# Kernel tuning notes

Hardware: AMD Instinct MI355X
Metric: run time of the kernel (lower is better)

## Reference

```python
import jax, jax.numpy as jnp
import numpy as np

EMBED_DIM = 1024
NUM_HEADS = 16
HEAD_DIM = EMBED_DIM // NUM_HEADS
SCALING = HEAD_DIM ** -0.5
W_SCALE = 0.02  # small init so exp(scores) in focused path stays finite


def setup_inputs() -> dict:
    key = jax.random.key(0)
    ks = jax.random.split(key, 12)
    B, T = 2, 2048
    hidden_states = jax.random.normal(ks[0], (B, T, EMBED_DIM), dtype=jnp.float32)
    focused_attention = jax.random.uniform(ks[1], (B, T, T), dtype=jnp.float32)
    def lin(kw, kb):
        W = jax.random.normal(kw, (EMBED_DIM, EMBED_DIM), dtype=jnp.float32) * W_SCALE
        b = jax.random.normal(kb, (EMBED_DIM,), dtype=jnp.float32) * W_SCALE
        return W, b
    Wq, bq = lin(ks[2], ks[3])
    Wk, bk = lin(ks[4], ks[5])
    Wv, bv = lin(ks[6], ks[7])
    Wo, bo = lin(ks[8], ks[9])
    return {"hidden_states": hidden_states, "focused_attention": focused_attention,
            "Wq": Wq, "bq": bq, "Wk": Wk, "bk": bk, "Wv": Wv, "bv": bv, "Wo": Wo, "bo": bo}


def reference(hidden_states, focused_attention, Wq, bq, Wk, bk, Wv, bv, Wo, bo):
    B, T, D = hidden_states.shape
    H, hd = NUM_HEADS, HEAD_DIM

    def shape_heads(x):  # [B,T,D] -> [B,H,T,hd]
        return x.reshape(B, T, H, hd).transpose(0, 2, 1, 3)

    q = shape_heads((hidden_states @ Wq.T + bq) * SCALING)
    k = shape_heads(hidden_states @ Wk.T + bk)
    v = shape_heads(hidden_states @ Wv.T + bv)

    # [B,H,T,S] raw attention logits
    scores = jnp.einsum('bhtd,bhsd->bhts', q, k)

    # focused_attention path: exp-weighted normalization (not a plain softmax)
    f = focused_attention[:, None, :, :]  # broadcast over heads
    e = f * jnp.exp(scores)
    attn = e / jnp.sum(e, axis=-1, keepdims=True)

    out = jnp.einsum('bhts,bhsd->bhtd', attn, v)  # [B,H,T,hd]
    out = out.transpose(0, 2, 1, 3).reshape(B, T, D)
    return out @ Wo.T + bo
```

## Files before the change

### kernel.cpp

```cpp
#include <hip/hip_runtime.h>
#include <stdint.h>


typedef __attribute__((ext_vector_type(8))) short short8;
typedef __attribute__((ext_vector_type(4))) short short4v;
typedef __attribute__((ext_vector_type(4))) float f32x4;
typedef unsigned short u16;

#define T_SEQ 2048
#define NH    16
#define HD    64
#define DM    1024

__device__ __forceinline__ float b2f(u16 h) {
  union { unsigned u; float f; } v; v.u = ((unsigned)h) << 16; return v.f;
}
__device__ __forceinline__ u16 f2bf(float x) {
  union { float f; unsigned u; } v; v.f = x;
  unsigned r = v.u + 0x7fffu + ((v.u >> 16) & 1u);
  return (u16)(r >> 16);
}
__device__ __forceinline__ unsigned pack_trunc(float a, float b) {
  union { float f; unsigned u; } ua, ub; ua.f = a; ub.f = b;
  return __builtin_amdgcn_perm(ub.u, ua.u, 0x07060302u);
}
__device__ __forceinline__ short8 cvt8(const float* p) {
  const f32x4 a = *(const f32x4*)p;
  const f32x4 b = *(const f32x4*)(p + 4);
  short8 o;
  o[0] = (short)f2bf(a[0]); o[1] = (short)f2bf(a[1]);
  o[2] = (short)f2bf(a[2]); o[3] = (short)f2bf(a[3]);
  o[4] = (short)f2bf(b[0]); o[5] = (short)f2bf(b[1]);
  o[6] = (short)f2bf(b[2]); o[7] = (short)f2bf(b[3]);
  return o;
}
__device__ __forceinline__ void gl_lds16(const void* g, void* l) {
  __builtin_amdgcn_global_load_lds(
      (const __attribute__((address_space(1))) void*)g,
      (__attribute__((address_space(3))) void*)l, 16, 0, 0);
}

#define QSCALE 0.18033688011112042f

#define HS_CH 524288u
#define F_CH  1048576u
#define W_CH  131072u
__global__ void cvt_kernel(const float* __restrict__ hs, const float* __restrict__ f,
                           const float* __restrict__ Wq, const float* __restrict__ Wk,
                           const float* __restrict__ Wv, const float* __restrict__ Wo,
                           u16* __restrict__ hsb, u16* __restrict__ fb,
                           u16* __restrict__ Wqb, u16* __restrict__ Wkb,
                           u16* __restrict__ Wvb, u16* __restrict__ Wob) {
  unsigned c = blockIdx.x * 256 + threadIdx.x;
  const float* s; u16* d; unsigned off;
  if (c < HS_CH)                       { s = hs; d = hsb; off = c; }
  else if ((c -= HS_CH) < F_CH)        { s = f;  d = fb;  off = c; }
  else if ((c -= F_CH) < W_CH)         { s = Wq; d = Wqb; off = c; }
  else if ((c -= W_CH) < W_CH)         { s = Wk; d = Wkb; off = c; }
  else if ((c -= W_CH) < W_CH)         { s = Wv; d = Wvb; off = c; }
  else                                 { s = Wo; d = Wob; off = c - W_CH; }
  *(short8*)&d[(size_t)off * 8] = cvt8(&s[(size_t)off * 8]);
}

__global__ __launch_bounds__(256, 4) void qkv_kernel(
    const void* __restrict__ Xv,
    const void* __restrict__ Wqv, const float* __restrict__ bq,
    const void* __restrict__ Wkv, const float* __restrict__ bk,
    const void* __restrict__ Wvv, const float* __restrict__ bv,
    int isf32,
    u16* __restrict__ q, u16* __restrict__ k, u16* __restrict__ v)
{
  const int z = blockIdx.z;
  const void* Wp = (z == 0) ? Wqv : (z == 1) ? Wkv : Wvv;
  const float* bias = (z == 0) ? bq : (z == 1) ? bk : bv;

  __shared__ alignas(16) u16 smem[16384];
  u16* lsA = smem;
  u16* lsB = smem + 8192;

  const int tid = threadIdx.x;
  const int lane = tid & 63;
  const int wv = tid >> 6;
  const int lq = lane >> 4, li = lane & 15;
  const int wm = wv >> 1, wn = wv & 1;

  const int m0 = blockIdx.y * 128;
  const int n0 = blockIdx.x * 128;

  f32x4 acc[4][4];
#pragma unroll
  for (int i = 0; i < 4; i++)
#pragma unroll
    for (int j = 0; j < 4; j++) acc[i][j] = (f32x4){0.f, 0.f, 0.f, 0.f};

  for (int k0 = 0; k0 < DM; k0 += 64) {
    if (isf32) {
      const float* X32 = (const float*)Xv;
      const float* W32 = (const float*)Wp;
#pragma unroll
      for (int r = 0; r < 4; ++r) {
        const int idx = tid + 256 * r;
        const int row = idx >> 3, slab = idx & 7;
        *(short8*)&lsA[(slab * 128 + row) * 8] = cvt8(&X32[(size_t)(m0 + row) * DM + k0 + slab * 8]);
        *(short8*)&lsB[(slab * 128 + row) * 8] = cvt8(&W32[(size_t)(n0 + row) * DM + k0 + slab * 8]);
      }
    } else {
      const u16* X16 = (const u16*)Xv;
      const u16* W16 = (const u16*)Wp;
#pragma unroll
      for (int r = 0; r < 4; ++r) {
        const int slab = wv + (r >> 1) * 4;
        const int row = (r & 1) * 64 + lane;
        gl_lds16(&X16[(size_t)(m0 + row) * DM + k0 + slab * 8], &lsA[(slab * 128 + row) * 8]);
        gl_lds16(&W16[(size_t)(n0 + row) * DM + k0 + slab * 8], &lsB[(slab * 128 + row) * 8]);
      }
    }
    __syncthreads();
#pragma unroll
    for (int ks = 0; ks < 2; ++ks) {
      short8 af[4], bf[4];
      const int slab = ks * 4 + lq;
#pragma unroll
      for (int mt = 0; mt < 4; ++mt)
        af[mt] = *(const short8*)&lsA[(slab * 128 + wm * 64 + mt * 16 + li) * 8];
#pragma unroll
      for (int nt = 0; nt < 4; ++nt)
        bf[nt] = *(const short8*)&lsB[(slab * 128 + wn * 64 + nt * 16 + li) * 8];
#pragma unroll
      for (int mt = 0; mt < 4; ++mt)
#pragma unroll
        for (int nt = 0; nt < 4; ++nt)
          acc[mt][nt] = __builtin_amdgcn_mfma_f32_16x16x32_bf16(af[mt], bf[nt], acc[mt][nt], 0, 0, 0);
    }
    __syncthreads();
  }

  float bs[4];
#pragma unroll
  for (int nt = 0; nt < 4; ++nt) bs[nt] = bias[n0 + wn * 64 + nt * 16 + li];

  if (z != 2) {
    const float scale = (z == 0) ? QSCALE : 1.0f;
    u16* dst = (z == 0) ? q : k;
#pragma unroll
    for (int mt = 0; mt < 4; ++mt) {
      const int mbase = m0 + wm * 64 + mt * 16 + lq * 4;
#pragma unroll
      for (int nt = 0; nt < 4; ++nt) {
        const int n = n0 + wn * 64 + nt * 16 + li;
#pragma unroll
        for (int r = 0; r < 4; ++r)
          dst[(size_t)(mbase + r) * DM + n] = f2bf((acc[mt][nt][r] + bs[nt]) * scale);
      }
    }
  } else {
    const int b = m0 >> 11;
    const int t0 = m0 & (T_SEQ - 1);
#pragma unroll
    for (int p2 = 0; p2 < 2; ++p2) {
      __syncthreads();
      if (wn == p2) {
#pragma unroll
        for (int mt = 0; mt < 4; ++mt) {
          const int mcol = wm * 64 + mt * 16 + lq * 4;
#pragma unroll
          for (int nt = 0; nt < 4; ++nt) {
            const int nrow = nt * 16 + li;
            u16 pk[4];
#pragma unroll
            for (int r = 0; r < 4; ++r) pk[r] = f2bf(acc[mt][nt][r] + bs[nt]);
            *(short4v*)&smem[nrow * 136 + mcol] = *(const short4v*)pk;
          }
        }
      }
      __syncthreads();
#pragma unroll
      for (int p = 0; p < 4; ++p) {
        const int rrow = p * 16 + (tid >> 4);
        const int c = tid & 15;
        const short8 val = *(const short8*)&smem[rrow * 136 + c * 8];
        const int ng = n0 + p2 * 64 + rrow;
        const int h = ng >> 6, d = ng & 63;
        *(short8*)&v[((size_t)(b * NH + h) * HD + d) * T_SEQ + t0 + c * 8] = val;
      }
    }
  }
}

__global__ __launch_bounds__(256, 3) void attn_kernel(
    const u16* __restrict__ q, const u16* __restrict__ k,
    const u16* __restrict__ v, const void* __restrict__ fv,
    int isf32, u16* __restrict__ ao)
{
  __shared__ alignas(16) u16 Kl[2][4096];
  __shared__ alignas(16) u16 Vl[2][4096];
  __shared__ alignas(16) u16 Fl[2][4096];

  const int tid = threadIdx.x;
  const int w = tid >> 6;
  const int lane = tid & 63;
  const int lq = lane >> 4, li = lane & 15;

  const int t0 = blockIdx.x * 64;
  const int h = blockIdx.y;
  const int b = blockIdx.z;

  const u16* qh = q + (size_t)b * T_SEQ * DM + h * HD;
  const u16* kh = k + (size_t)b * T_SEQ * DM + h * HD;
  const u16* vh = v + (size_t)(b * NH + h) * HD * T_SEQ;
  const u16* f16p = (const u16*)fv + (size_t)b * T_SEQ * T_SEQ;
  const float* f32p = (const float*)fv + (size_t)b * T_SEQ * T_SEQ;

  short8 qf[2];
#pragma unroll
  for (int kk = 0; kk < 2; ++kk)
    qf[kk] = *(const short8*)&qh[(size_t)(t0 + w * 16 + li) * DM + kk * 32 + lq * 8];

  f32x4 oacc[4];
#pragma unroll
  for (int j = 0; j < 4; j++) oacc[j] = (f32x4){0.f, 0.f, 0.f, 0.f};
  float den = 0.f;

#define STAGE_KV(S0, BUF)                                                        \
  {                                                                              \
    _Pragma("unroll")                                                            \
    for (int r = 0; r < 2; ++r) {                                                \
      const int L = r * 256 + tid;                                               \
      const int row = L >> 3, jx = L & 7;                                        \
      const int j = jx ^ (row & 7);                                              \
      gl_lds16(kh + (size_t)((S0) + row) * DM + j * 8, &Kl[BUF][(size_t)L * 8]); \
      gl_lds16(vh + (size_t)row * T_SEQ + (S0) + j * 8, &Vl[BUF][(size_t)L * 8]);\
      if (!isf32)                                                                \
        gl_lds16(f16p + (size_t)(t0 + row) * T_SEQ + (S0) + j * 8,               \
                 &Fl[BUF][(size_t)L * 8]);                                       \
    }                                                                            \
  }

  STAGE_KV(0, 0)
  __syncthreads();

  for (int it = 0; it < 32; ++it) {
    const int cur = it & 1;
    const int s0 = it * 64;
    if (it < 31) STAGE_KV(s0 + 64, cur ^ 1)

    const u16* Kb = &Kl[cur][0];
    const u16* Vb = &Vl[cur][0];
    u16* Fb = &Fl[cur][0];

    short8 kf[2][4];
#pragma unroll
    for (int kk = 0; kk < 2; ++kk)
#pragma unroll
      for (int mt = 0; mt < 4; ++mt) {
        const int sl = mt * 16 + li;
        const int c = sl * 8 + ((kk * 4 + lq) ^ (sl & 7));
        kf[kk][mt] = *(const short8*)&Kb[(size_t)c * 8];
      }

    f32x4 sacc[4];
#pragma unroll
    for (int mt = 0; mt < 4; ++mt) sacc[mt] = (f32x4){0.f, 0.f, 0.f, 0.f};
#pragma unroll
    for (int kk = 0; kk < 2; ++kk)
#pragma unroll
      for (int mt = 0; mt < 4; ++mt)
        sacc[mt] = __builtin_amdgcn_mfma_f32_16x16x32_bf16(kf[kk][mt], qf[kk], sacc[mt], 0, 0, 0);

    const int trow = w * 16 + li;
#pragma unroll
    for (int mt = 0; mt < 4; ++mt) {
      const int cx = (mt * 2 + (lq >> 1)) ^ (trow & 7);
      u16* faddr = Fb + ((size_t)trow * 8 + cx) * 8 + (lq & 1) * 4;
      float p0, p1, p2, p3;
      if (isf32) {
        const f32x4 fx = *(const f32x4*)&f32p[(size_t)(t0 + trow) * T_SEQ + s0 + mt * 16 + lq * 4];
        p0 = fx[0] * __builtin_amdgcn_exp2f(sacc[mt][0]);
        p1 = fx[1] * __builtin_amdgcn_exp2f(sacc[mt][1]);
        p2 = fx[2] * __builtin_amdgcn_exp2f(sacc[mt][2]);
        p3 = fx[3] * __builtin_amdgcn_exp2f(sacc[mt][3]);
      } else {
        const short4v fr = *(const short4v*)faddr;
        p0 = b2f((u16)fr[0]) * __builtin_amdgcn_exp2f(sacc[mt][0]);
        p1 = b2f((u16)fr[1]) * __builtin_amdgcn_exp2f(sacc[mt][1]);
        p2 = b2f((u16)fr[2]) * __builtin_amdgcn_exp2f(sacc[mt][2]);
        p3 = b2f((u16)fr[3]) * __builtin_amdgcn_exp2f(sacc[mt][3]);
      }
      den += (p0 + p1) + (p2 + p3);
      unsigned lo = pack_trunc(p0, p1);
      unsigned hi = pack_trunc(p2, p3);
      union { unsigned u[2]; short4v s; } pv;
      pv.u[0] = lo; pv.u[1] = hi;
      *(short4v*)faddr = pv.s;
    }

#pragma unroll
    for (int kk = 0; kk < 2; ++kk) {
      const int cxp = ((kk * 4 + lq) ^ (trow & 7));
      const short8 pf = *(const short8*)&Fb[((size_t)trow * 8 + cxp) * 8];
#pragma unroll
      for (int dn = 0; dn < 4; ++dn) {
        const int d = dn * 16 + li;
        const int cv = d * 8 + ((kk * 4 + lq) ^ (d & 7));
        const short8 vf = *(const short8*)&Vb[(size_t)cv * 8];
        oacc[dn] = __builtin_amdgcn_mfma_f32_16x16x32_bf16(pf, vf, oacc[dn], 0, 0, 0);
      }
    }
    __syncthreads();
  }

  den += __shfl_xor(den, 16, 64);
  den += __shfl_xor(den, 32, 64);

  __syncthreads();
  u16* pw = &Kl[0][0] + w * 1152;
#pragma unroll
  for (int r = 0; r < 4; ++r) {
    const float rd = 1.0f / __shfl(den, lq * 4 + r, 64);
#pragma unroll
    for (int dn = 0; dn < 4; ++dn)
      pw[(lq * 4 + r) * 72 + dn * 16 + li] = f2bf(oacc[dn][r] * rd);
  }
#pragma unroll
  for (int p = 0; p < 2; ++p) {
    const int idx = p * 64 + lane;
    const int rloc = idx >> 3, c = idx & 7;
    const short8 vv = *(const short8*)&pw[rloc * 72 + c * 8];
    *(short8*)&ao[(size_t)(b * T_SEQ + t0 + w * 16 + rloc) * DM + h * HD + c * 8] = vv;
  }
#undef STAGE_KV
}

__global__ __launch_bounds__(256, 4) void oproj_kernel(
    const u16* __restrict__ A, const void* __restrict__ Wov,
    const float* __restrict__ bo, int isf32, float* __restrict__ out)
{
  __shared__ alignas(16) u16 smem[16384];
  u16* lsA = smem;
  u16* lsB = smem + 8192;

  const int tid = threadIdx.x;
  const int lane = tid & 63;
  const int wv = tid >> 6;
  const int lq = lane >> 4, li = lane & 15;
  const int wm = wv >> 1, wn = wv & 1;

  const int m0 = blockIdx.y * 128;
  const int n0 = blockIdx.x * 128;

  f32x4 acc[4][4];
#pragma unroll
  for (int i = 0; i < 4; i++)
#pragma unroll
    for (int j = 0; j < 4; j++) acc[i][j] = (f32x4){0.f, 0.f, 0.f, 0.f};

  for (int k0 = 0; k0 < DM; k0 += 64) {
#pragma unroll
    for (int r = 0; r < 4; ++r) {
      const int slab = wv + (r >> 1) * 4;
      const int row = (r & 1) * 64 + lane;
      gl_lds16(&A[(size_t)(m0 + row) * DM + k0 + slab * 8], &lsA[(slab * 128 + row) * 8]);
    }
    if (isf32) {
      const float* W32 = (const float*)Wov;
#pragma unroll
      for (int r = 0; r < 4; ++r) {
        const int idx = tid + 256 * r;
        const int row = idx >> 3, slab = idx & 7;
        *(short8*)&lsB[(slab * 128 + row) * 8] = cvt8(&W32[(size_t)(n0 + row) * DM + k0 + slab * 8]);
      }
    } else {
      const u16* W16 = (const u16*)Wov;
#pragma unroll
      for (int r = 0; r < 4; ++r) {
        const int slab = wv + (r >> 1) * 4;
        const int row = (r & 1) * 64 + lane;
        gl_lds16(&W16[(size_t)(n0 + row) * DM + k0 + slab * 8], &lsB[(slab * 128 + row) * 8]);
      }
    }
    __syncthreads();
#pragma unroll
    for (int ks = 0; ks < 2; ++ks) {
      short8 af[4], bf[4];
      const int slab = ks * 4 + lq;
#pragma unroll
      for (int mt = 0; mt < 4; ++mt)
        af[mt] = *(const short8*)&lsA[(slab * 128 + wm * 64 + mt * 16 + li) * 8];
#pragma unroll
      for (int nt = 0; nt < 4; ++nt)
        bf[nt] = *(const short8*)&lsB[(slab * 128 + wn * 64 + nt * 16 + li) * 8];
#pragma unroll
      for (int mt = 0; mt < 4; ++mt)
#pragma unroll
        for (int nt = 0; nt < 4; ++nt)
          acc[mt][nt] = __builtin_amdgcn_mfma_f32_16x16x32_bf16(af[mt], bf[nt], acc[mt][nt], 0, 0, 0);
    }
    __syncthreads();
  }

  float bs[4];
#pragma unroll
  for (int nt = 0; nt < 4; ++nt) bs[nt] = bo[n0 + wn * 64 + nt * 16 + li];

#pragma unroll
  for (int mt = 0; mt < 4; ++mt) {
    const int mbase = m0 + wm * 64 + mt * 16 + lq * 4;
#pragma unroll
    for (int nt = 0; nt < 4; ++nt) {
      const int n = n0 + wn * 64 + nt * 16 + li;
#pragma unroll
      for (int r = 0; r < 4; ++r)
        out[(size_t)(mbase + r) * DM + n] = acc[mt][nt][r] + bs[nt];
    }
  }
}

extern "C" void kernel_launch(void* const* d_in, const int* in_sizes, int n_in,
                              void* d_out, int out_size, void* d_ws, size_t ws_size,
                              hipStream_t stream) {
  (void)in_sizes; (void)n_in; (void)out_size;
  const float* hs = (const float*)d_in[0];
  const float* fa = (const float*)d_in[1];
  const float* Wq = (const float*)d_in[2];
  const float* bq = (const float*)d_in[3];
  const float* Wk = (const float*)d_in[4];
  const float* bk = (const float*)d_in[5];
  const float* Wv = (const float*)d_in[6];
  const float* bv = (const float*)d_in[7];
  const float* Wo = (const float*)d_in[8];
  const float* bo = (const float*)d_in[9];
  float* out = (float*)d_out;

  const size_t NEED = 256 + 2u * (8388608u + 4194304u + 4u * 1048576u + 4u * 4194304u);
  char* base = (char*)d_ws + 256;
  if (ws_size >= NEED) {
    u16* fb  = (u16*)base;
    u16* hsb = fb + 8388608u;
    u16* Wqb = hsb + 4194304u;
    u16* Wkb = Wqb + 1048576u;
    u16* Wvb = Wkb + 1048576u;
    u16* Wob = Wvb + 1048576u;
    u16* qw  = Wob + 1048576u;
    u16* kw  = qw + 4194304u;
    u16* vw  = kw + 4194304u;
    u16* aw  = vw + 4194304u;
    cvt_kernel<<<8192, 256, 0, stream>>>(hs, fa, Wq, Wk, Wv, Wo, hsb, fb, Wqb, Wkb, Wvb, Wob);
    qkv_kernel<<<dim3(8, 32, 3), 256, 0, stream>>>(hsb, Wqb, bq, Wkb, bk, Wvb, bv, 0, qw, kw, vw);
    attn_kernel<<<dim3(32, 16, 2), 256, 0, stream>>>(qw, kw, vw, fb, 0, aw);
    oproj_kernel<<<dim3(8, 32, 1), 256, 0, stream>>>(aw, Wob, bo, 0, out);
  } else {
    u16* qw = (u16*)base;
    u16* kw = qw + 4194304u;
    u16* vw = kw + 4194304u;
    u16* aw = vw + 4194304u;
    qkv_kernel<<<dim3(8, 32, 3), 256, 0, stream>>>(hs, Wq, bq, Wk, bk, Wv, bv, 1, qw, kw, vw);
    attn_kernel<<<dim3(32, 16, 2), 256, 0, stream>>>(qw, kw, vw, fa, 1, aw);
    oproj_kernel<<<dim3(8, 32, 1), 256, 0, stream>>>(aw, Wo, bo, 1, out);
  }
}
```

Baseline: 293.2 us.

## Shrink GEMM tiles and single-buffer F staging to raise occupancy

The QKV projection tile shrinks from 128x128 to 64x128, and the output projection tile shrinks from 128x128 to 64x64. The V-transpose epilogue is rewritten as a single pass, and grids and launch bounds are enlarged so more blocks run per CU and there are more waves. In the attention kernel the focused-attention tile moves out of the double-buffered K/V staging into a single per-iteration buffer loaded at the start of each step, cutting LDS so occupancy can go from 3 to 4 blocks. The trade-off is less data reuse per block in the GEMMs and an unprefetched F load in attention, which may expose memory latency.

```diff
diff --git a/kernel.cpp b/kernel.cpp
--- a/kernel.cpp
+++ b/kernel.cpp
@@ -62,7 +62,7 @@
   *(short8*)&d[(size_t)off * 8] = cvt8(&s[(size_t)off * 8]);
 }
 
-__global__ __launch_bounds__(256, 4) void qkv_kernel(
+__global__ __launch_bounds__(256, 5) void qkv_kernel(
     const void* __restrict__ Xv,
     const void* __restrict__ Wqv, const float* __restrict__ bq,
     const void* __restrict__ Wkv, const float* __restrict__ bk,
@@ -74,9 +74,9 @@
   const void* Wp = (z == 0) ? Wqv : (z == 1) ? Wkv : Wvv;
   const float* bias = (z == 0) ? bq : (z == 1) ? bk : bv;
 
-  __shared__ alignas(16) u16 smem[16384];
+  __shared__ alignas(16) u16 smem[12288];
   u16* lsA = smem;
-  u16* lsB = smem + 8192;
+  u16* lsB = smem + 4096;
 
   const int tid = threadIdx.x;
   const int lane = tid & 63;
@@ -84,12 +84,12 @@
   const int lq = lane >> 4, li = lane & 15;
   const int wm = wv >> 1, wn = wv & 1;
 
-  const int m0 = blockIdx.y * 128;
+  const int m0 = blockIdx.y * 64;
   const int n0 = blockIdx.x * 128;
 
-  f32x4 acc[4][4];
-#pragma unroll
-  for (int i = 0; i < 4; i++)
+  f32x4 acc[2][4];
+#pragma unroll
+  for (int i = 0; i < 2; i++)
 #pragma unroll
     for (int j = 0; j < 4; j++) acc[i][j] = (f32x4){0.f, 0.f, 0.f, 0.f};
 
@@ -98,36 +98,45 @@
       const float* X32 = (const float*)Xv;
       const float* W32 = (const float*)Wp;
 #pragma unroll
+      for (int r = 0; r < 2; ++r) {
+        const int idx = tid + 256 * r;
+        const int row = idx >> 3, slab = idx & 7;
+        *(short8*)&lsA[(slab * 64 + row) * 8] = cvt8(&X32[(size_t)(m0 + row) * DM + k0 + slab * 8]);
+      }
+#pragma unroll
       for (int r = 0; r < 4; ++r) {
         const int idx = tid + 256 * r;
         const int row = idx >> 3, slab = idx & 7;
-        *(short8*)&lsA[(slab * 128 + row) * 8] = cvt8(&X32[(size_t)(m0 + row) * DM + k0 + slab * 8]);
         *(short8*)&lsB[(slab * 128 + row) * 8] = cvt8(&W32[(size_t)(n0 + row) * DM + k0 + slab * 8]);
       }
     } else {
       const u16* X16 = (const u16*)Xv;
       const u16* W16 = (const u16*)Wp;
 #pragma unroll
+      for (int r = 0; r < 2; ++r) {
+        const int slab = wv * 2 + r;
+        gl_lds16(&X16[(size_t)(m0 + lane) * DM + k0 + slab * 8], &lsA[(slab * 64 + lane) * 8]);
+      }
+#pragma unroll
       for (int r = 0; r < 4; ++r) {
-        const int slab = wv + (r >> 1) * 4;
+        const int slab = wv * 2 + (r >> 1);
         const int row = (r & 1) * 64 + lane;
-        gl_lds16(&X16[(size_t)(m0 + row) * DM + k0 + slab * 8], &lsA[(slab * 128 + row) * 8]);
         gl_lds16(&W16[(size_t)(n0 + row) * DM + k0 + slab * 8], &lsB[(slab * 128 + row) * 8]);
       }
     }
     __syncthreads();
 #pragma unroll
     for (int ks = 0; ks < 2; ++ks) {
-      short8 af[4], bf[4];
       const int slab = ks * 4 + lq;
-#pragma unroll
-      for (int mt = 0; mt < 4; ++mt)
-        af[mt] = *(const short8*)&lsA[(slab * 128 + wm * 64 + mt * 16 + li) * 8];
+      short8 af[2], bf[4];
+#pragma unroll
+      for (int mt = 0; mt < 2; ++mt)
+        af[mt] = *(const short8*)&lsA[(slab * 64 + wm * 32 + mt * 16 + li) * 8];
 #pragma unroll
       for (int nt = 0; nt < 4; ++nt)
         bf[nt] = *(const short8*)&lsB[(slab * 128 + wn * 64 + nt * 16 + li) * 8];
 #pragma unroll
-      for (int mt = 0; mt < 4; ++mt)
+      for (int mt = 0; mt < 2; ++mt)
 #pragma unroll
         for (int nt = 0; nt < 4; ++nt)
           acc[mt][nt] = __builtin_amdgcn_mfma_f32_16x16x32_bf16(af[mt], bf[nt], acc[mt][nt], 0, 0, 0);
@@ -143,8 +152,8 @@
     const float scale = (z == 0) ? QSCALE : 1.0f;
     u16* dst = (z == 0) ? q : k;
 #pragma unroll
-    for (int mt = 0; mt < 4; ++mt) {
-      const int mbase = m0 + wm * 64 + mt * 16 + lq * 4;
+    for (int mt = 0; mt < 2; ++mt) {
+      const int mbase = m0 + wm * 32 + mt * 16 + lq * 4;
 #pragma unroll
       for (int nt = 0; nt < 4; ++nt) {
         const int n = n0 + wn * 64 + nt * 16 + li;
@@ -155,46 +164,40 @@
     }
   } else {
     const int b = m0 >> 11;
-    const int t0 = m0 & (T_SEQ - 1);
-#pragma unroll
-    for (int p2 = 0; p2 < 2; ++p2) {
-      __syncthreads();
-      if (wn == p2) {
-#pragma unroll
-        for (int mt = 0; mt < 4; ++mt) {
-          const int mcol = wm * 64 + mt * 16 + lq * 4;
-#pragma unroll
-          for (int nt = 0; nt < 4; ++nt) {
-            const int nrow = nt * 16 + li;
-            u16 pk[4];
-#pragma unroll
-            for (int r = 0; r < 4; ++r) pk[r] = f2bf(acc[mt][nt][r] + bs[nt]);
-            *(short4v*)&smem[nrow * 136 + mcol] = *(const short4v*)pk;
-          }
-        }
-      }
-      __syncthreads();
-#pragma unroll
-      for (int p = 0; p < 4; ++p) {
-        const int rrow = p * 16 + (tid >> 4);
-        const int c = tid & 15;
-        const short8 val = *(const short8*)&smem[rrow * 136 + c * 8];
-        const int ng = n0 + p2 * 64 + rrow;
-        const int h = ng >> 6, d = ng & 63;
-        *(short8*)&v[((size_t)(b * NH + h) * HD + d) * T_SEQ + t0 + c * 8] = val;
-      }
-    }
-  }
-}
-
-__global__ __launch_bounds__(256, 3) void attn_kernel(
+    const int t0g = m0 & (T_SEQ - 1);
+#pragma unroll
+    for (int mt = 0; mt < 2; ++mt) {
+      const int mcol = wm * 32 + mt * 16 + lq * 4;
+#pragma unroll
+      for (int nt = 0; nt < 4; ++nt) {
+        const int nrow = wn * 64 + nt * 16 + li;
+        u16 pk[4];
+#pragma unroll
+        for (int r = 0; r < 4; ++r) pk[r] = f2bf(acc[mt][nt][r] + bs[nt]);
+        *(short4v*)&smem[nrow * 72 + mcol] = *(const short4v*)pk;
+      }
+    }
+    __syncthreads();
+#pragma unroll
+    for (int p = 0; p < 4; ++p) {
+      const int idx = p * 256 + tid;
+      const int nrow = idx >> 3, c = idx & 7;
+      const short8 val = *(const short8*)&smem[nrow * 72 + c * 8];
+      const int ng = n0 + nrow;
+      const int h = ng >> 6, d = ng & 63;
+      *(short8*)&v[((size_t)(b * NH + h) * HD + d) * T_SEQ + t0g + c * 8] = val;
+    }
+  }
+}
+
+__global__ __launch_bounds__(256, 4) void attn_kernel(
     const u16* __restrict__ q, const u16* __restrict__ k,
     const u16* __restrict__ v, const void* __restrict__ fv,
     int isf32, u16* __restrict__ ao)
 {
   __shared__ alignas(16) u16 Kl[2][4096];
   __shared__ alignas(16) u16 Vl[2][4096];
-  __shared__ alignas(16) u16 Fl[2][4096];
+  __shared__ alignas(16) u16 Fl[4096];
 
   const int tid = threadIdx.x;
   const int w = tid >> 6;
@@ -230,9 +233,19 @@
       const int j = jx ^ (row & 7);                                              \
       gl_lds16(kh + (size_t)((S0) + row) * DM + j * 8, &Kl[BUF][(size_t)L * 8]); \
       gl_lds16(vh + (size_t)row * T_SEQ + (S0) + j * 8, &Vl[BUF][(size_t)L * 8]);\
-      if (!isf32)                                                                \
-        gl_lds16(f16p + (size_t)(t0 + row) * T_SEQ + (S0) + j * 8,               \
-                 &Fl[BUF][(size_t)L * 8]);                                       \
+    }                                                                            \
+  }
+
+#define STAGE_F(S0)                                                              \
+  {                                                                              \
+    _Pragma("unroll")                                                            \
+    for (int r = 0; r < 2; ++r) {                                                \
+      const int Ll = r * 64 + lane;                      \
+      const int row = w * 16 + (Ll >> 3);                                        \
+      const int cx = Ll & 7;                                                     \
+      const int j = cx ^ (row & 7);                                              \
+      gl_lds16(f16p + (size_t)(t0 + row) * T_SEQ + (S0) + j * 8,                 \
+               &Fl[((size_t)w * 128 + Ll) * 8]);                                 \
     }                                                                            \
   }
 
@@ -242,11 +255,11 @@
   for (int it = 0; it < 32; ++it) {
     const int cur = it & 1;
     const int s0 = it * 64;
+    if (!isf32) STAGE_F(s0)
     if (it < 31) STAGE_KV(s0 + 64, cur ^ 1)
 
     const u16* Kb = &Kl[cur][0];
     const u16* Vb = &Vl[cur][0];
-    u16* Fb = &Fl[cur][0];
 
     short8 kf[2][4];
 #pragma unroll
@@ -271,7 +284,7 @@
 #pragma unroll
     for (int mt = 0; mt < 4; ++mt) {
       const int cx = (mt * 2 + (lq >> 1)) ^ (trow & 7);
-      u16* faddr = Fb + ((size_t)trow * 8 + cx) * 8 + (lq & 1) * 4;
+      u16* faddr = Fl + ((size_t)trow * 8 + cx) * 8 + (lq & 1) * 4;
       float p0, p1, p2, p3;
       if (isf32) {
         const f32x4 fx = *(const f32x4*)&f32p[(size_t)(t0 + trow) * T_SEQ + s0 + mt * 16 + lq * 4];
@@ -287,17 +300,16 @@
         p3 = b2f((u16)fr[3]) * __builtin_amdgcn_exp2f(sacc[mt][3]);
       }
       den += (p0 + p1) + (p2 + p3);
-      unsigned lo = pack_trunc(p0, p1);
-      unsigned hi = pack_trunc(p2, p3);
       union { unsigned u[2]; short4v s; } pv;
-      pv.u[0] = lo; pv.u[1] = hi;
+      pv.u[0] = pack_trunc(p0, p1);
+      pv.u[1] = pack_trunc(p2, p3);
       *(short4v*)faddr = pv.s;
     }
 
 #pragma unroll
     for (int kk = 0; kk < 2; ++kk) {
       const int cxp = ((kk * 4 + lq) ^ (trow & 7));
-      const short8 pf = *(const short8*)&Fb[((size_t)trow * 8 + cxp) * 8];
+      const short8 pf = *(const short8*)&Fl[((size_t)trow * 8 + cxp) * 8];
 #pragma unroll
       for (int dn = 0; dn < 4; ++dn) {
         const int d = dn * 16 + li;
@@ -329,15 +341,16 @@
     *(short8*)&ao[(size_t)(b * T_SEQ + t0 + w * 16 + rloc) * DM + h * HD + c * 8] = vv;
   }
 #undef STAGE_KV
+#undef STAGE_F
 }
 
 __global__ __launch_bounds__(256, 4) void oproj_kernel(
     const u16* __restrict__ A, const void* __restrict__ Wov,
     const float* __restrict__ bo, int isf32, float* __restrict__ out)
 {
-  __shared__ alignas(16) u16 smem[16384];
+  __shared__ alignas(16) u16 smem[8192];
   u16* lsA = smem;
-  u16* lsB = smem + 8192;
+  u16* lsB = smem + 4096;
 
   const int tid = threadIdx.x;
   const int lane = tid & 63;
@@ -345,69 +358,67 @@
   const int lq = lane >> 4, li = lane & 15;
   const int wm = wv >> 1, wn = wv & 1;
 
-  const int m0 = blockIdx.y * 128;
-  const int n0 = blockIdx.x * 128;
-
-  f32x4 acc[4][4];
-#pragma unroll
-  for (int i = 0; i < 4; i++)
-#pragma unroll
-    for (int j = 0; j < 4; j++) acc[i][j] = (f32x4){0.f, 0.f, 0.f, 0.f};
+  const int m0 = blockIdx.y * 64;
+  const int n0 = blockIdx.x * 64;
+
+  f32x4 acc[2][2];
+#pragma unroll
+  for (int i = 0; i < 2; i++)
+#pragma unroll
+    for (int j = 0; j < 2; j++) acc[i][j] = (f32x4){0.f, 0.f, 0.f, 0.f};
 
   for (int k0 = 0; k0 < DM; k0 += 64) {
 #pragma unroll
-    for (int r = 0; r < 4; ++r) {
-      const int slab = wv + (r >> 1) * 4;
-      const int row = (r & 1) * 64 + lane;
-      gl_lds16(&A[(size_t)(m0 + row) * DM + k0 + slab * 8], &lsA[(slab * 128 + row) * 8]);
+    for (int r = 0; r < 2; ++r) {
+      const int slab = wv * 2 + r;
+      gl_lds16(&A[(size_t)(m0 + lane) * DM + k0 + slab * 8], &lsA[(slab * 64 + lane) * 8]);
     }
     if (isf32) {
       const float* W32 = (const float*)Wov;
 #pragma unroll
-      for (int r = 0; r < 4; ++r) {
+      for (int r = 0; r < 2; ++r) {
         const int idx = tid + 256 * r;
         const int row = idx >> 3, slab = idx & 7;
-        *(short8*)&lsB[(slab * 128 + row) * 8] = cvt8(&W32[(size_t)(n0 + row) * DM + k0 + slab * 8]);
+        *(short8*)&lsB[(slab * 64 + row) * 8] = cvt8(&W32[(size_t)(n0 + row) * DM + k0 + slab * 8]);
       }
     } else {
       const u16* W16 = (const u16*)Wov;
 #pragma unroll
-      for (int r = 0; r < 4; ++r) {
-        const int slab = wv + (r >> 1) * 4;
-        const int row = (r & 1) * 64 + lane;
-        gl_lds16(&W16[(size_t)(n0 + row) * DM + k0 + slab * 8], &lsB[(slab * 128 + row) * 8]);
+      for (int r = 0; r < 2; ++r) {
+        const int slab = wv * 2 + r;
+        gl_lds16(&W16[(size_t)(n0 + lane) * DM + k0 + slab * 8], &lsB[(slab * 64 + lane) * 8]);
       }
     }
     __syncthreads();
 #pragma unroll
     for (int ks = 0; ks < 2; ++ks) {
-      short8 af[4], bf[4];
       const int slab = ks * 4 + lq;
-#pragma unroll
-      for (int mt = 0; mt < 4; ++mt)
-        af[mt] = *(const short8*)&lsA[(slab * 128 + wm * 64 + mt * 16 + li) * 8];
-#pragma unroll
-      for (int nt = 0; nt < 4; ++nt)
-        bf[nt] = *(const short8*)&lsB[(slab * 128 + wn * 64 + nt * 16 + li) * 8];
-#pragma unroll
-      for (int mt = 0; mt < 4; ++mt)
-#pragma unroll
-        for (int nt = 0; nt < 4; ++nt)
+      short8 af[2], bf[2];
+#pragma unroll
+      for (int mt = 0; mt < 2; ++mt)
+        af[mt] = *(const short8*)&lsA[(slab * 64 + wm * 32 + mt * 16 + li) * 8];
+#pragma unroll
+      for (int nt = 0; nt < 2; ++nt)
+        bf[nt] = *(const short8*)&lsB[(slab * 64 + wn * 32 + nt * 16 + li) * 8];
+#pragma unroll
+      for (int mt = 0; mt < 2; ++mt)
+#pragma unroll
+        for (int nt = 0; nt < 2; ++nt)
           acc[mt][nt] = __builtin_amdgcn_mfma_f32_16x16x32_bf16(af[mt], bf[nt], acc[mt][nt], 0, 0, 0);
     }
     __syncthreads();
   }
 
-  float bs[4];
-#pragma unroll
-  for (int nt = 0; nt < 4; ++nt) bs[nt] = bo[n0 + wn * 64 + nt * 16 + li];
-
-#pragma unroll
-  for (int mt = 0; mt < 4; ++mt) {
-    const int mbase = m0 + wm * 64 + mt * 16 + lq * 4;
-#pragma unroll
-    for (int nt = 0; nt < 4; ++nt) {
-      const int n = n0 + wn * 64 + nt * 16 + li;
+  float bs[2];
+#pragma unroll
+  for (int nt = 0; nt < 2; ++nt) bs[nt] = bo[n0 + wn * 32 + nt * 16 + li];
+
+#pragma unroll
+  for (int mt = 0; mt < 2; ++mt) {
+    const int mbase = m0 + wm * 32 + mt * 16 + lq * 4;
+#pragma unroll
+    for (int nt = 0; nt < 2; ++nt) {
+      const int n = n0 + wn * 32 + nt * 16 + li;
 #pragma unroll
       for (int r = 0; r < 4; ++r)
         out[(size_t)(mbase + r) * DM + n] = acc[mt][nt][r] + bs[nt];
@@ -445,16 +456,16 @@
     u16* vw  = kw + 4194304u;
     u16* aw  = vw + 4194304u;
     cvt_kernel<<<8192, 256, 0, stream>>>(hs, fa, Wq, Wk, Wv, Wo, hsb, fb, Wqb, Wkb, Wvb, Wob);
-    qkv_kernel<<<dim3(8, 32, 3), 256, 0, stream>>>(hsb, Wqb, bq, Wkb, bk, Wvb, bv, 0, qw, kw, vw);
+    qkv_kernel<<<dim3(8, 64, 3), 256, 0, stream>>>(hsb, Wqb, bq, Wkb, bk, Wvb, bv, 0, qw, kw, vw);
     attn_kernel<<<dim3(32, 16, 2), 256, 0, stream>>>(qw, kw, vw, fb, 0, aw);
-    oproj_kernel<<<dim3(8, 32, 1), 256, 0, stream>>>(aw, Wob, bo, 0, out);
+    oproj_kernel<<<dim3(16, 64), 256, 0, stream>>>(aw, Wob, bo, 0, out);
   } else {
     u16* qw = (u16*)base;
     u16* kw = qw + 4194304u;
     u16* vw = kw + 4194304u;
     u16* aw = vw + 4194304u;
-    qkv_kernel<<<dim3(8, 32, 3), 256, 0, stream>>>(hs, Wq, bq, Wk, bk, Wv, bv, 1, qw, kw, vw);
+    qkv_kernel<<<dim3(8, 64, 3), 256, 0, stream>>>(hs, Wq, bq, Wk, bk, Wv, bv, 1, qw, kw, vw);
     attn_kernel<<<dim3(32, 16, 2), 256, 0, stream>>>(qw, kw, vw, fa, 1, aw);
-    oproj_kernel<<<dim3(8, 32, 1), 256, 0, stream>>>(aw, Wo, bo, 1, out);
-  }
-}
+    oproj_kernel<<<dim3(16, 64), 256, 0, stream>>>(aw, Wo, bo, 1, out);
+  }
+}
```

Result: slower. 304.5 us (+3.8%).
